# Optimization experiments

Hardware: AMD Instinct MI355X
Metric: run time of the kernel (lower is better)

The kernel has to match this reference:

```python
import jax, jax.numpy as jnp
import numpy as np

N, K, P_DIM, HID, NCLS = 20000, 16, 63, 32 + 0, 32
HID = 128
IN_DIM = P_DIM + 1


def setup_inputs() -> dict:
    key = jax.random.key(0)
    ks = iter(jax.random.split(key, 64))

    def nrm(shape, s=0.1):
        return jax.random.normal(next(ks), shape, jnp.float32) * s

    inp = {
        "p": nrm((N, P_DIM), 1.0),
        "neigh_idx": jax.random.randint(next(ks), (N, K), 0, N, dtype=jnp.int32),
    }
    dims = [(IN_DIM, HID), (HID, HID), (HID, NCLS)]
    for l, (din, dout) in enumerate(dims):
        inp[f"l{l}_Wih"] = nrm((4 * din, din))
        inp[f"l{l}_Whh"] = nrm((4 * din, din))
        inp[f"l{l}_bih"] = jnp.zeros((4 * din,), jnp.float32)
        inp[f"l{l}_bhh"] = jnp.zeros((4 * din,), jnp.float32)
        inp[f"l{l}_Wself"] = nrm((dout, din))
        inp[f"l{l}_Wneigh"] = nrm((dout, din))
        inp[f"l{l}_b"] = jnp.zeros((dout,), jnp.float32)
    return inp


def _lstm_agg(feat, neigh_idx, Wih, Whh, bih, bhh):
    # Per-node LSTM over the K in-neighbor features (DGL _lstm_reducer).
    n, h_dim = feat.shape[0], Whh.shape[1]
    bias = bih + bhh

    def step(carry, idx_t):
        h, c = carry
        x = feat[idx_t]                                   # [N, Din] gather (step t message)
        g = x @ Wih.T + h @ Whh.T + bias                  # [N, 4H]
        i, f, gg, o = jnp.split(g, 4, axis=-1)            # torch LSTM gate order i,f,g,o
        c = jax.nn.sigmoid(f) * c + jax.nn.sigmoid(i) * jnp.tanh(gg)
        h = jax.nn.sigmoid(o) * jnp.tanh(c)
        return (h, c), None

    init = (jnp.zeros((n, h_dim), feat.dtype), jnp.zeros((n, h_dim), feat.dtype))
    (h, _), _ = jax.lax.scan(step, init, neigh_idx.T)     # scan over K neighbor slots
    return h                                              # final hidden state = neigh feat


def _forward(p, neigh_idx, *params):
    # features = cat(in_degree/N, p); fixed-degree graph -> in_degree == K
    deg = jnp.full((p.shape[0], 1), K / N, p.dtype)
    feat = jnp.concatenate([deg, p], axis=1)
    layers = [params[7 * l: 7 * (l + 1)] for l in range(3)]
    for l, (Wih, Whh, bih, bhh, Wself, Wneigh, b) in enumerate(layers):
        neigh = _lstm_agg(feat, neigh_idx, Wih, Whh, bih, bhh)
        feat = feat @ Wself.T + neigh @ Wneigh.T + b      # fc_self + fc_neigh + bias
        if l < 2:
            feat = jax.nn.relu(feat)
    return feat


def reference(p, neigh_idx,
              l0_Wih, l0_Whh, l0_bih, l0_bhh, l0_Wself, l0_Wneigh, l0_b,
              l1_Wih, l1_Whh, l1_bih, l1_bhh, l1_Wself, l1_Wneigh, l1_b,
              l2_Wih, l2_Whh, l2_bih, l2_bhh, l2_Wself, l2_Wneigh, l2_b):
    return _forward(p, neigh_idx,
                    l0_Wih, l0_Whh, l0_bih, l0_bhh, l0_Wself, l0_Wneigh, l0_b,
                    l1_Wih, l1_Whh, l1_bih, l1_bhh, l1_Wself, l1_Wneigh, l1_b,
                    l2_Wih, l2_Whh, l2_bih, l2_bhh, l2_Wself, l2_Wneigh, l2_b)
```

## Files before the change

### kernel.cpp

```cpp
#include <hip/hip_runtime.h>
#include <hip/hip_bf16.h>
#include <stdint.h>


#define N_NODES 20000
#define KNE 16
#define C1F 1.442695041f
#define C2F 2.885390082f

typedef __bf16 bf16x8 __attribute__((ext_vector_type(8)));
typedef float f32x4 __attribute__((ext_vector_type(4)));

__device__ __forceinline__ bf16x8 ldb8(const __hip_bfloat16* p) {
  uint4 u = *reinterpret_cast<const uint4*>(p);
  return __builtin_bit_cast(bf16x8, u);
}
__device__ __forceinline__ void pin(bf16x8& v) {
  uint4 u = __builtin_bit_cast(uint4, v);
  asm volatile("" : "+v"(u.x), "+v"(u.y), "+v"(u.z), "+v"(u.w));
  v = __builtin_bit_cast(bf16x8, u);
}
__device__ __forceinline__ float b2f_lo(uint32_t u) {
  return __builtin_bit_cast(float, u << 16);
}
__device__ __forceinline__ float b2f_hi(uint32_t u) {
  return __builtin_bit_cast(float, u & 0xffff0000u);
}
__device__ __forceinline__ uint32_t pk2(float a, float b) {
  uint32_t ua = (uint32_t)__builtin_bit_cast(unsigned short, __float2bfloat16(a));
  uint32_t ub = (uint32_t)__builtin_bit_cast(unsigned short, __float2bfloat16(b));
  return ua | (ub << 16);
}

struct CvtArgs {
  const float* s[12];
  __hip_bfloat16* d[12];
  int off[13];
  int gsz[12];
};
__global__ void cvt_all(CvtArgs a) {
  int i = blockIdx.x * 256 + threadIdx.x;
  if (i >= a.off[12]) return;
#pragma unroll
  for (int k = 0; k < 12; ++k)
    if (i >= a.off[k] && i < a.off[k + 1]) {
      int j = i - a.off[k];
      float v = a.s[k][j];
      if (a.gsz[k]) {
        int g = j / a.gsz[k];
        v *= (g == 2) ? C2F : -C1F;
      }
      a.d[k][j] = __float2bfloat16(v);
    }
}

template <int DIN, int DOUT, int NTR, int WW>
__device__ __forceinline__ void proj_phase(
    const __hip_bfloat16* sA,
    const __hip_bfloat16* __restrict__ Wih,
    const float* __restrict__ bih, const float* __restrict__ bhh,
    const __hip_bfloat16* __restrict__ Wself,
    const float* __restrict__ bvec,
    __hip_bfloat16* __restrict__ P, float* __restrict__ S,
    int n0, int wv, int quad, int c16) {
  constexpr int KB = DIN / 32;
  constexpr int CCT = DIN / 16;
  constexpr int CTS = DOUT / 16;
  constexpr int HS = DIN + 8;
  const f32x4 zz = {0.f, 0.f, 0.f, 0.f};
  bf16x8 afr[NTR][KB];
#pragma unroll
  for (int nt = 0; nt < NTR; ++nt)
#pragma unroll
    for (int kb = 0; kb < KB; ++kb)
      afr[nt][kb] = ldb8(&sA[(nt * 16 + c16) * HS + kb * 32 + quad * 8]);

  for (int ct = wv; ct < CCT + CTS; ct += WW) {
    if (ct < CCT) {
      const int cc = ct * 16 + c16;
      f32x4 ag[4][NTR];
#pragma unroll
      for (int g = 0; g < 4; ++g)
#pragma unroll
        for (int nt = 0; nt < NTR; ++nt) ag[g][nt] = zz;
#pragma unroll
      for (int kb = 0; kb < KB; ++kb)
#pragma unroll
        for (int g = 0; g < 4; ++g) {
          bf16x8 b =
              ldb8(Wih + (size_t)(g * DIN + cc) * DIN + kb * 32 + quad * 8);
#pragma unroll
          for (int nt = 0; nt < NTR; ++nt)
            ag[g][nt] = __builtin_amdgcn_mfma_f32_16x16x32_bf16(
                afr[nt][kb], b, ag[g][nt], 0, 0, 0);
        }
      float bi = -C1F * (bih[cc] + bhh[cc]);
      float bf_ = -C1F * (bih[DIN + cc] + bhh[DIN + cc]);
      float bg = C2F * (bih[2 * DIN + cc] + bhh[2 * DIN + cc]);
      float bo = -C1F * (bih[3 * DIN + cc] + bhh[3 * DIN + cc]);
      uint2* Pp = reinterpret_cast<uint2*>(P);
#pragma unroll
      for (int nt = 0; nt < NTR; ++nt)
#pragma unroll
        for (int r = 0; r < 4; ++r) {
          int n = n0 + nt * 16 + quad * 4 + r;
          uint2 u;
          u.x = pk2(ag[0][nt][r] + bi, ag[1][nt][r] + bf_);
          u.y = pk2(ag[2][nt][r] + bg, ag[3][nt][r] + bo);
          Pp[(size_t)n * DIN + cc] = u;
        }
    } else {
      const int c = (ct - CCT) * 16 + c16;
      f32x4 a[NTR];
#pragma unroll
      for (int nt = 0; nt < NTR; ++nt) a[nt] = zz;
#pragma unroll
      for (int kb = 0; kb < KB; ++kb) {
        bf16x8 b = ldb8(Wself + (size_t)c * DIN + kb * 32 + quad * 8);
#pragma unroll
        for (int nt = 0; nt < NTR; ++nt)
          a[nt] = __builtin_amdgcn_mfma_f32_16x16x32_bf16(afr[nt][kb], b,
                                                          a[nt], 0, 0, 0);
      }
      float bias = bvec[c];
#pragma unroll
      for (int nt = 0; nt < NTR; ++nt)
#pragma unroll
        for (int r = 0; r < 4; ++r)
          S[(size_t)(n0 + nt * 16 + quad * 4 + r) * DOUT + c] =
              a[nt][r] + bias;
    }
  }
}

__global__ __launch_bounds__(256, 2) void feat_proj0(
    const float* __restrict__ p,
    const __hip_bfloat16* __restrict__ Wih,
    const float* __restrict__ bih, const float* __restrict__ bhh,
    const __hip_bfloat16* __restrict__ Wself,
    const float* __restrict__ bvec,
    __hip_bfloat16* __restrict__ P, float* __restrict__ S) {
  __shared__ __align__(16) __hip_bfloat16 sFeat[32 * 72];
  const int n0 = blockIdx.x * 32;
  const int tid = threadIdx.x;
  const int wv = tid >> 6;
  const int lane = tid & 63;
  const int quad = lane >> 4;
  const int c16 = lane & 15;

  for (int i = tid; i < 32 * 64; i += 256) {
    int n = i >> 6, c = i & 63;
    float v = (c == 0) ? ((float)KNE / (float)N_NODES)
                       : p[(size_t)(n0 + n) * 63 + c - 1];
    sFeat[n * 72 + c] = __float2bfloat16(v);
  }
  __syncthreads();
  proj_phase<64, 128, 2, 4>(sFeat, Wih, bih, bhh, Wself, bvec, P, S, n0, wv,
                            quad, c16);
}

template <int DIN, int DOUT, int DOUTN, int NT, bool RELU>
__global__ __launch_bounds__((DIN / 16) * 64)
__attribute__((amdgpu_waves_per_eu(4))) void lstm_proj_kern(
    const __hip_bfloat16* __restrict__ P,
    const float* __restrict__ S,
    const __hip_bfloat16* __restrict__ Whh,
    const __hip_bfloat16* __restrict__ Wng,
    const int* __restrict__ nidx,
    const __hip_bfloat16* __restrict__ Wih2,
    const float* __restrict__ bih2, const float* __restrict__ bhh2,
    const __hip_bfloat16* __restrict__ Wself2,
    const float* __restrict__ bvec2,
    __hip_bfloat16* __restrict__ P2, float* __restrict__ S2) {
  constexpr int W = DIN / 16;
  constexpr int KB = DIN / 32;
  constexpr int HS = DIN + 8;
  constexpr int NN = 16 * NT;
  constexpr int HS2 = DOUT + 8;

  __shared__ __align__(16) __hip_bfloat16 hl[2][NN * HS];
  __shared__ __align__(16) __hip_bfloat16 sOut[NN * HS2];
  __shared__ int idxl[NN * KNE];

  const int n0 = blockIdx.x * NN;
  const int tid = threadIdx.x;
  const int wv = tid >> 6;
  const int lane = tid & 63;
  const int quad = lane >> 4;
  const int c16 = lane & 15;
  const int col = wv * 16 + c16;

  for (int i = tid; i < NN * KNE; i += W * 64) idxl[i] = nidx[n0 * KNE + i];
  __syncthreads();

  uint2 pf[2][NT][4];
  auto loadpf = [&](int t, int b) {
#pragma unroll
    for (int nt = 0; nt < NT; ++nt)
#pragma unroll
      for (int r = 0; r < 4; ++r) {
        int src = idxl[(nt * 16 + quad * 4 + r) * KNE + t];
        pf[b][nt][r] =
            reinterpret_cast<const uint2*>(P + (size_t)src * (4 * DIN))[col];
      }
  };

  loadpf(0, 0);

  bf16x8 Bp[4][KB];
#pragma unroll
  for (int g = 0; g < 4; ++g)
#pragma unroll
    for (int kb = 0; kb < KB; ++kb) {
      Bp[g][kb] =
          ldb8(Whh + (size_t)(g * DIN + col) * DIN + kb * 32 + quad * 8);
      pin(Bp[g][kb]);
    }

  loadpf(1, 1);

  float cst[NT][4];
#pragma unroll
  for (int nt = 0; nt < NT; ++nt)
#pragma unroll
    for (int r = 0; r < 4; ++r) cst[nt][r] = 0.f;

  auto initag = [&](int b, int nt, f32x4 (&ag)[4]) {
#pragma unroll
    for (int r = 0; r < 4; ++r) {
      ag[0][r] = b2f_lo(pf[b][nt][r].x);
      ag[1][r] = b2f_hi(pf[b][nt][r].x);
      ag[2][r] = b2f_lo(pf[b][nt][r].y);
      ag[3][r] = b2f_hi(pf[b][nt][r].y);
    }
  };

  auto gates = [&](int hb, int nt, const f32x4 (&ag)[4]) {
#pragma unroll
    for (int r = 0; r < 4; ++r) {
      float wi = __builtin_amdgcn_rcpf(1.f + __builtin_amdgcn_exp2f(ag[0][r]));
      float wf = __builtin_amdgcn_rcpf(1.f + __builtin_amdgcn_exp2f(ag[1][r]));
      float wg = __builtin_amdgcn_rcpf(1.f + __builtin_amdgcn_exp2f(ag[2][r]));
      float wo = __builtin_amdgcn_rcpf(1.f + __builtin_amdgcn_exp2f(ag[3][r]));
      float tg = fmaf(-2.f, wg, 1.f);
      float cc = wf * cst[nt][r] + wi * tg;
      cst[nt][r] = cc;
      float tc = fmaf(
          -2.f,
          __builtin_amdgcn_rcpf(1.f + __builtin_amdgcn_exp2f(C2F * cc)), 1.f);
      hl[hb][(nt * 16 + quad * 4 + r) * HS + col] =
          __float2bfloat16(wo * tc);
    }
  };

#pragma unroll
  for (int nt = 0; nt < NT; ++nt) {
    f32x4 ag[4];
    initag(0, nt, ag);
    gates(0, nt, ag);
  }

#pragma unroll
  for (int t = 1; t < KNE; ++t) {
    __syncthreads();
    if (t + 1 < KNE) loadpf(t + 1, (t + 1) & 1);
    const int pb = (t - 1) & 1;
#pragma unroll
    for (int nt = 0; nt < NT; ++nt) {
      bf16x8 Af[KB];
#pragma unroll
      for (int kb = 0; kb < KB; ++kb)
        Af[kb] = ldb8(&hl[pb][(nt * 16 + c16) * HS + kb * 32 + quad * 8]);
      f32x4 ag[4];
      initag(t & 1, nt, ag);
#pragma unroll
      for (int kb = 0; kb < KB; ++kb)
#pragma unroll
        for (int g = 0; g < 4; ++g)
          ag[g] = __builtin_amdgcn_mfma_f32_16x16x32_bf16(Af[kb], Bp[g][kb],
                                                          ag[g], 0, 0, 0);
      gates(t & 1, nt, ag);
    }
  }

  const f32x4 zz = {0.f, 0.f, 0.f, 0.f};
  __syncthreads();
  bf16x8 Hf[NT][KB];
#pragma unroll
  for (int nt = 0; nt < NT; ++nt)
#pragma unroll
    for (int kb = 0; kb < KB; ++kb)
      Hf[nt][kb] = ldb8(&hl[1][(nt * 16 + c16) * HS + kb * 32 + quad * 8]);
  for (int ct = wv; ct < DOUT / 16; ct += W) {
    f32x4 a[NT];
#pragma unroll
    for (int nt = 0; nt < NT; ++nt) a[nt] = zz;
#pragma unroll
    for (int kb = 0; kb < KB; ++kb) {
      bf16x8 b = ldb8(Wng + (size_t)(ct * 16 + c16) * DIN + kb * 32 + quad * 8);
#pragma unroll
      for (int nt = 0; nt < NT; ++nt)
        a[nt] = __builtin_amdgcn_mfma_f32_16x16x32_bf16(Hf[nt][kb], b, a[nt],
                                                        0, 0, 0);
    }
#pragma unroll
    for (int nt = 0; nt < NT; ++nt)
#pragma unroll
      for (int r = 0; r < 4; ++r) {
        int n = n0 + nt * 16 + quad * 4 + r;
        int c = ct * 16 + c16;
        float v = a[nt][r] + S[(size_t)n * DOUT + c];
        if (RELU) v = fmaxf(v, 0.f);
        sOut[(nt * 16 + quad * 4 + r) * HS2 + c] = __float2bfloat16(v);
      }
  }
  __syncthreads();
  proj_phase<DOUT, DOUTN, NT, W>(sOut, Wih2, bih2, bhh2, Wself2, bvec2, P2,
                                 S2, n0, wv, quad, c16);
}

template <int DIN, int DOUT>
__global__ __launch_bounds__((DIN / 16) * 64)
__attribute__((amdgpu_waves_per_eu(4))) void lstm_out_kern(
    const __hip_bfloat16* __restrict__ P, const float* __restrict__ S,
    const __hip_bfloat16* __restrict__ Whh,
    const __hip_bfloat16* __restrict__ Wng, const int* __restrict__ nidx,
    float* __restrict__ outp) {
  constexpr int W = DIN / 16;
  constexpr int KB = DIN / 32;
  constexpr int HS = DIN + 8;

  __shared__ __align__(16) __hip_bfloat16 hl[2][16 * HS];
  __shared__ int idxl[16 * KNE];

  const int n0 = blockIdx.x * 16;
  const int tid = threadIdx.x;
  const int wv = tid >> 6;
  const int lane = tid & 63;
  const int quad = lane >> 4;
  const int c16 = lane & 15;
  const int col = wv * 16 + c16;

  for (int i = tid; i < 16 * KNE; i += W * 64) idxl[i] = nidx[n0 * KNE + i];
  __syncthreads();

  uint2 pf[2][4];
  auto loadpf = [&](int t, int b) {
#pragma unroll
    for (int r = 0; r < 4; ++r) {
      int src = idxl[(quad * 4 + r) * KNE + t];
      pf[b][r] =
          reinterpret_cast<const uint2*>(P + (size_t)src * (4 * DIN))[col];
    }
  };

  loadpf(0, 0);
  bf16x8 Bp[4][KB];
#pragma unroll
  for (int g = 0; g < 4; ++g)
#pragma unroll
    for (int kb = 0; kb < KB; ++kb) {
      Bp[g][kb] =
          ldb8(Whh + (size_t)(g * DIN + col) * DIN + kb * 32 + quad * 8);
      pin(Bp[g][kb]);
    }
  loadpf(1, 1);

  float cst[4];
#pragma unroll
  for (int r = 0; r < 4; ++r) cst[r] = 0.f;

  auto initag = [&](int b, f32x4 (&ag)[4]) {
#pragma unroll
    for (int r = 0; r < 4; ++r) {
      ag[0][r] = b2f_lo(pf[b][r].x);
      ag[1][r] = b2f_hi(pf[b][r].x);
      ag[2][r] = b2f_lo(pf[b][r].y);
      ag[3][r] = b2f_hi(pf[b][r].y);
    }
  };
  auto gates = [&](int hb, const f32x4 (&ag)[4]) {
#pragma unroll
    for (int r = 0; r < 4; ++r) {
      float wi = __builtin_amdgcn_rcpf(1.f + __builtin_amdgcn_exp2f(ag[0][r]));
      float wf = __builtin_amdgcn_rcpf(1.f + __builtin_amdgcn_exp2f(ag[1][r]));
      float wg = __builtin_amdgcn_rcpf(1.f + __builtin_amdgcn_exp2f(ag[2][r]));
      float wo = __builtin_amdgcn_rcpf(1.f + __builtin_amdgcn_exp2f(ag[3][r]));
      float tg = fmaf(-2.f, wg, 1.f);
      float cc = wf * cst[r] + wi * tg;
      cst[r] = cc;
      float tc = fmaf(
          -2.f,
          __builtin_amdgcn_rcpf(1.f + __builtin_amdgcn_exp2f(C2F * cc)), 1.f);
      hl[hb][(quad * 4 + r) * HS + col] = __float2bfloat16(wo * tc);
    }
  };

  {
    f32x4 ag[4];
    initag(0, ag);
    gates(0, ag);
  }
#pragma unroll
  for (int t = 1; t < KNE; ++t) {
    __syncthreads();
    if (t + 1 < KNE) loadpf(t + 1, (t + 1) & 1);
    const int pb = (t - 1) & 1;
    bf16x8 Af[KB];
#pragma unroll
    for (int kb = 0; kb < KB; ++kb)
      Af[kb] = ldb8(&hl[pb][c16 * HS + kb * 32 + quad * 8]);
    f32x4 ag[4];
    initag(t & 1, ag);
#pragma unroll
    for (int kb = 0; kb < KB; ++kb)
#pragma unroll
      for (int g = 0; g < 4; ++g)
        ag[g] = __builtin_amdgcn_mfma_f32_16x16x32_bf16(Af[kb], Bp[g][kb],
                                                        ag[g], 0, 0, 0);
    gates(t & 1, ag);
  }

  const f32x4 zz = {0.f, 0.f, 0.f, 0.f};
  __syncthreads();
  bf16x8 Hf[KB];
#pragma unroll
  for (int kb = 0; kb < KB; ++kb)
    Hf[kb] = ldb8(&hl[1][c16 * HS + kb * 32 + quad * 8]);
  for (int ct = wv; ct < DOUT / 16; ct += W) {
    f32x4 a = zz;
#pragma unroll
    for (int kb = 0; kb < KB; ++kb) {
      bf16x8 b = ldb8(Wng + (size_t)(ct * 16 + c16) * DIN + kb * 32 + quad * 8);
      a = __builtin_amdgcn_mfma_f32_16x16x32_bf16(Hf[kb], b, a, 0, 0, 0);
    }
#pragma unroll
    for (int r = 0; r < 4; ++r) {
      int n = n0 + quad * 4 + r;
      int c = ct * 16 + c16;
      outp[(size_t)n * DOUT + c] = a[r] + S[(size_t)n * DOUT + c];
    }
  }
}

extern "C" void kernel_launch(void* const* d_in, const int* in_sizes, int n_in,
                              void* d_out, int out_size, void* d_ws,
                              size_t ws_size, hipStream_t stream) {
  (void)in_sizes; (void)n_in; (void)out_size; (void)ws_size;
  const float* p = (const float*)d_in[0];
  const int* nidx = (const int*)d_in[1];
  const float* L[3][7];
  for (int l = 0; l < 3; ++l)
    for (int j = 0; j < 7; ++j)
      L[l][j] = (const float*)d_in[2 + 7 * l + j];

  char* w = (char*)d_ws;
  __hip_bfloat16* P0 = (__hip_bfloat16*)(w);
  float*          S0 = (float*)(w + 10240000);
  __hip_bfloat16* P1 = (__hip_bfloat16*)(w + 20480000);
  float*          S1 = (float*)(w + 40960000);
  float*          S2 = (float*)(w + 51200000);
  __hip_bfloat16* P2 = (__hip_bfloat16*)(w);
  __hip_bfloat16* wb = (__hip_bfloat16*)(w + 53760000);

  const int din_[3] = {64, 128, 128}, dout_[3] = {128, 128, 32};
  __hip_bfloat16 *Wih_b[3], *Whh_b[3], *Wself_b[3], *Wng_b[3];
  CvtArgs ca;
  size_t off = 0;
  int k = 0, pre = 0;
  for (int l = 0; l < 3; ++l) {
    int din = din_[l], dout = dout_[l];
    int n0 = 4 * din * din, n2 = dout * din;
    Wih_b[l] = wb + off;   off += (size_t)n0;
    Whh_b[l] = wb + off;   off += (size_t)n0;
    Wself_b[l] = wb + off; off += (size_t)n2;
    Wng_b[l] = wb + off;   off += (size_t)n2;
    const float* srcs[4] = {L[l][0], L[l][1], L[l][4], L[l][5]};
    __hip_bfloat16* dsts[4] = {Wih_b[l], Whh_b[l], Wself_b[l], Wng_b[l]};
    int ns[4] = {n0, n0, n2, n2};
    int gs[4] = {din * din, din * din, 0, 0};
    for (int j = 0; j < 4; ++j) {
      ca.s[k] = srcs[j];
      ca.d[k] = dsts[j];
      ca.off[k] = pre;
      ca.gsz[k] = gs[j];
      pre += ns[j];
      ++k;
    }
  }
  ca.off[12] = pre;

  cvt_all<<<(pre + 255) / 256, 256, 0, stream>>>(ca);

  feat_proj0<<<N_NODES / 32, 256, 0, stream>>>(
      p, Wih_b[0], L[0][2], L[0][3], Wself_b[0], L[0][6], P0, S0);

  lstm_proj_kern<64, 128, 128, 2, true><<<N_NODES / 32, 256, 0, stream>>>(
      P0, S0, Whh_b[0], Wng_b[0], nidx, Wih_b[1], L[1][2], L[1][3],
      Wself_b[1], L[1][6], P1, S1);

  lstm_proj_kern<128, 128, 32, 1, true><<<N_NODES / 16, 512, 0, stream>>>(
      P1, S1, Whh_b[1], Wng_b[1], nidx, Wih_b[2], L[2][2], L[2][3],
      Wself_b[2], L[2][6], P2, S2);

  lstm_out_kern<128, 32><<<N_NODES / 16, 512, 0, stream>>>(
      P2, S2, Whh_b[2], Wng_b[2], nidx, (float*)d_out);
}
```

Before: 327.3 us.

## Widen per-wave column tiles and stream Whh from cache in 128-dim LSTM kernels

```diff
diff --git a/kernel.cpp b/kernel.cpp
--- a/kernel.cpp
+++ b/kernel.cpp
@@ -159,8 +159,9 @@
                             quad, c16);
 }
 
-template <int DIN, int DOUT, int DOUTN, int NT, bool RELU>
-__global__ __launch_bounds__((DIN / 16) * 64)
+template <int DIN, int DOUT, int DOUTN, int NT, int CW, bool STREAMB,
+          bool RELU>
+__global__ __launch_bounds__((DIN / CW) * 64)
 __attribute__((amdgpu_waves_per_eu(4))) void lstm_proj_kern(
     const __hip_bfloat16* __restrict__ P,
     const float* __restrict__ S,
@@ -172,7 +173,8 @@
     const __hip_bfloat16* __restrict__ Wself2,
     const float* __restrict__ bvec2,
     __hip_bfloat16* __restrict__ P2, float* __restrict__ S2) {
-  constexpr int W = DIN / 16;
+  constexpr int W = DIN / CW;
+  constexpr int JJ = CW / 16;
   constexpr int KB = DIN / 32;
   constexpr int HS = DIN + 8;
   constexpr int NN = 16 * NT;
@@ -188,54 +190,63 @@
   const int lane = tid & 63;
   const int quad = lane >> 4;
   const int c16 = lane & 15;
-  const int col = wv * 16 + c16;
 
   for (int i = tid; i < NN * KNE; i += W * 64) idxl[i] = nidx[n0 * KNE + i];
   __syncthreads();
 
-  uint2 pf[2][NT][4];
+  uint2 pf[2][NT][JJ][4];
   auto loadpf = [&](int t, int b) {
 #pragma unroll
     for (int nt = 0; nt < NT; ++nt)
 #pragma unroll
       for (int r = 0; r < 4; ++r) {
         int src = idxl[(nt * 16 + quad * 4 + r) * KNE + t];
-        pf[b][nt][r] =
-            reinterpret_cast<const uint2*>(P + (size_t)src * (4 * DIN))[col];
+        const uint2* bp =
+            reinterpret_cast<const uint2*>(P + (size_t)src * (4 * DIN));
+#pragma unroll
+        for (int jj = 0; jj < JJ; ++jj)
+          pf[b][nt][jj][r] = bp[wv * CW + jj * 16 + c16];
       }
   };
 
   loadpf(0, 0);
 
-  bf16x8 Bp[4][KB];
-#pragma unroll
-  for (int g = 0; g < 4; ++g)
-#pragma unroll
-    for (int kb = 0; kb < KB; ++kb) {
-      Bp[g][kb] =
-          ldb8(Whh + (size_t)(g * DIN + col) * DIN + kb * 32 + quad * 8);
-      pin(Bp[g][kb]);
-    }
+  bf16x8 Bp[STREAMB ? 1 : 4][STREAMB ? 1 : JJ][STREAMB ? 1 : KB];
+  if constexpr (!STREAMB) {
+#pragma unroll
+    for (int g = 0; g < 4; ++g)
+#pragma unroll
+      for (int jj = 0; jj < JJ; ++jj)
+#pragma unroll
+        for (int kb = 0; kb < KB; ++kb) {
+          Bp[g][jj][kb] =
+              ldb8(Whh + (size_t)(g * DIN + wv * CW + jj * 16 + c16) * DIN +
+                   kb * 32 + quad * 8);
+          pin(Bp[g][jj][kb]);
+        }
+  }
 
   loadpf(1, 1);
 
-  float cst[NT][4];
+  float cst[NT][JJ][4];
 #pragma unroll
   for (int nt = 0; nt < NT; ++nt)
 #pragma unroll
-    for (int r = 0; r < 4; ++r) cst[nt][r] = 0.f;
-
-  auto initag = [&](int b, int nt, f32x4 (&ag)[4]) {
+    for (int jj = 0; jj < JJ; ++jj)
+#pragma unroll
+      for (int r = 0; r < 4; ++r) cst[nt][jj][r] = 0.f;
+
+  auto initag = [&](int b, int nt, int jj, f32x4 (&ag)[4]) {
 #pragma unroll
     for (int r = 0; r < 4; ++r) {
-      ag[0][r] = b2f_lo(pf[b][nt][r].x);
-      ag[1][r] = b2f_hi(pf[b][nt][r].x);
-      ag[2][r] = b2f_lo(pf[b][nt][r].y);
-      ag[3][r] = b2f_hi(pf[b][nt][r].y);
+      ag[0][r] = b2f_lo(pf[b][nt][jj][r].x);
+      ag[1][r] = b2f_hi(pf[b][nt][jj][r].x);
+      ag[2][r] = b2f_lo(pf[b][nt][jj][r].y);
+      ag[3][r] = b2f_hi(pf[b][nt][jj][r].y);
     }
   };
 
-  auto gates = [&](int hb, int nt, const f32x4 (&ag)[4]) {
+  auto gates = [&](int hb, int nt, int jj, const f32x4 (&ag)[4]) {
 #pragma unroll
     for (int r = 0; r < 4; ++r) {
       float wi = __builtin_amdgcn_rcpf(1.f + __builtin_amdgcn_exp2f(ag[0][r]));
@@ -243,43 +254,62 @@
       float wg = __builtin_amdgcn_rcpf(1.f + __builtin_amdgcn_exp2f(ag[2][r]));
       float wo = __builtin_amdgcn_rcpf(1.f + __builtin_amdgcn_exp2f(ag[3][r]));
       float tg = fmaf(-2.f, wg, 1.f);
-      float cc = wf * cst[nt][r] + wi * tg;
-      cst[nt][r] = cc;
+      float cc = wf * cst[nt][jj][r] + wi * tg;
+      cst[nt][jj][r] = cc;
       float tc = fmaf(
           -2.f,
           __builtin_amdgcn_rcpf(1.f + __builtin_amdgcn_exp2f(C2F * cc)), 1.f);
-      hl[hb][(nt * 16 + quad * 4 + r) * HS + col] =
+      hl[hb][(nt * 16 + quad * 4 + r) * HS + wv * CW + jj * 16 + c16] =
           __float2bfloat16(wo * tc);
     }
   };
 
 #pragma unroll
-  for (int nt = 0; nt < NT; ++nt) {
-    f32x4 ag[4];
-    initag(0, nt, ag);
-    gates(0, nt, ag);
-  }
+  for (int nt = 0; nt < NT; ++nt)
+#pragma unroll
+    for (int jj = 0; jj < JJ; ++jj) {
+      f32x4 ag[4];
+      initag(0, nt, jj, ag);
+      gates(0, nt, jj, ag);
+    }
 
 #pragma unroll
   for (int t = 1; t < KNE; ++t) {
     __syncthreads();
     if (t + 1 < KNE) loadpf(t + 1, (t + 1) & 1);
     const int pb = (t - 1) & 1;
+    const __hip_bfloat16* Wt = Whh;
+    if constexpr (STREAMB) {
+      int toff = 0;
+      asm volatile("" : "+s"(toff));
+      Wt = Whh + toff;
+    }
 #pragma unroll
     for (int nt = 0; nt < NT; ++nt) {
       bf16x8 Af[KB];
 #pragma unroll
       for (int kb = 0; kb < KB; ++kb)
         Af[kb] = ldb8(&hl[pb][(nt * 16 + c16) * HS + kb * 32 + quad * 8]);
-      f32x4 ag[4];
-      initag(t & 1, nt, ag);
-#pragma unroll
-      for (int kb = 0; kb < KB; ++kb)
-#pragma unroll
-        for (int g = 0; g < 4; ++g)
-          ag[g] = __builtin_amdgcn_mfma_f32_16x16x32_bf16(Af[kb], Bp[g][kb],
-                                                          ag[g], 0, 0, 0);
-      gates(t & 1, nt, ag);
+#pragma unroll
+      for (int jj = 0; jj < JJ; ++jj) {
+        f32x4 ag[4];
+        initag(t & 1, nt, jj, ag);
+#pragma unroll
+        for (int kb = 0; kb < KB; ++kb)
+#pragma unroll
+          for (int g = 0; g < 4; ++g) {
+            bf16x8 b;
+            if constexpr (STREAMB)
+              b = ldb8(Wt +
+                       (size_t)(g * DIN + wv * CW + jj * 16 + c16) * DIN +
+                       kb * 32 + quad * 8);
+            else
+              b = Bp[g][jj][kb];
+            ag[g] = __builtin_amdgcn_mfma_f32_16x16x32_bf16(Af[kb], b, ag[g],
+                                                            0, 0, 0);
+          }
+        gates(t & 1, nt, jj, ag);
+      }
     }
   }
 
@@ -319,14 +349,15 @@
                                  S2, n0, wv, quad, c16);
 }
 
-template <int DIN, int DOUT>
-__global__ __launch_bounds__((DIN / 16) * 64)
+template <int DIN, int DOUT, int CW, bool STREAMB>
+__global__ __launch_bounds__((DIN / CW) * 64)
 __attribute__((amdgpu_waves_per_eu(4))) void lstm_out_kern(
     const __hip_bfloat16* __restrict__ P, const float* __restrict__ S,
     const __hip_bfloat16* __restrict__ Whh,
     const __hip_bfloat16* __restrict__ Wng, const int* __restrict__ nidx,
     float* __restrict__ outp) {
-  constexpr int W = DIN / 16;
+  constexpr int W = DIN / CW;
+  constexpr int JJ = CW / 16;
   constexpr int KB = DIN / 32;
   constexpr int HS = DIN + 8;
 
@@ -339,47 +370,58 @@
   const int lane = tid & 63;
   const int quad = lane >> 4;
   const int c16 = lane & 15;
-  const int col = wv * 16 + c16;
 
   for (int i = tid; i < 16 * KNE; i += W * 64) idxl[i] = nidx[n0 * KNE + i];
   __syncthreads();
 
-  uint2 pf[2][4];
+  uint2 pf[2][JJ][4];
   auto loadpf = [&](int t, int b) {
 #pragma unroll
     for (int r = 0; r < 4; ++r) {
       int src = idxl[(quad * 4 + r) * KNE + t];
-      pf[b][r] =
-          reinterpret_cast<const uint2*>(P + (size_t)src * (4 * DIN))[col];
+      const uint2* bp =
+          reinterpret_cast<const uint2*>(P + (size_t)src * (4 * DIN));
+#pragma unroll
+      for (int jj = 0; jj < JJ; ++jj)
+        pf[b][jj][r] = bp[wv * CW + jj * 16 + c16];
     }
   };
 
   loadpf(0, 0);
-  bf16x8 Bp[4][KB];
-#pragma unroll
-  for (int g = 0; g < 4; ++g)
-#pragma unroll
-    for (int kb = 0; kb < KB; ++kb) {
-      Bp[g][kb] =
-          ldb8(Whh + (size_t)(g * DIN + col) * DIN + kb * 32 + quad * 8);
-      pin(Bp[g][kb]);
-    }
+
+  bf16x8 Bp[STREAMB ? 1 : 4][STREAMB ? 1 : JJ][STREAMB ? 1 : KB];
+  if constexpr (!STREAMB) {
+#pragma unroll
+    for (int g = 0; g < 4; ++g)
+#pragma unroll
+      for (int jj = 0; jj < JJ; ++jj)
+#pragma unroll
+        for (int kb = 0; kb < KB; ++kb) {
+          Bp[g][jj][kb] =
+              ldb8(Whh + (size_t)(g * DIN + wv * CW + jj * 16 + c16) * DIN +
+                   kb * 32 + quad * 8);
+          pin(Bp[g][jj][kb]);
+        }
+  }
+
   loadpf(1, 1);
 
-  float cst[4];
-#pragma unroll
-  for (int r = 0; r < 4; ++r) cst[r] = 0.f;
-
-  auto initag = [&](int b, f32x4 (&ag)[4]) {
+  float cst[JJ][4];
+#pragma unroll
+  for (int jj = 0; jj < JJ; ++jj)
+#pragma unroll
+    for (int r = 0; r < 4; ++r) cst[jj][r] = 0.f;
+
+  auto initag = [&](int b, int jj, f32x4 (&ag)[4]) {
 #pragma unroll
     for (int r = 0; r < 4; ++r) {
-      ag[0][r] = b2f_lo(pf[b][r].x);
-      ag[1][r] = b2f_hi(pf[b][r].x);
-      ag[2][r] = b2f_lo(pf[b][r].y);
-      ag[3][r] = b2f_hi(pf[b][r].y);
+      ag[0][r] = b2f_lo(pf[b][jj][r].x);
+      ag[1][r] = b2f_hi(pf[b][jj][r].x);
+      ag[2][r] = b2f_lo(pf[b][jj][r].y);
+      ag[3][r] = b2f_hi(pf[b][jj][r].y);
     }
   };
-  auto gates = [&](int hb, const f32x4 (&ag)[4]) {
+  auto gates = [&](int hb, int jj, const f32x4 (&ag)[4]) {
 #pragma unroll
     for (int r = 0; r < 4; ++r) {
       float wi = __builtin_amdgcn_rcpf(1.f + __builtin_amdgcn_exp2f(ag[0][r]));
@@ -387,38 +429,57 @@
       float wg = __builtin_amdgcn_rcpf(1.f + __builtin_amdgcn_exp2f(ag[2][r]));
       float wo = __builtin_amdgcn_rcpf(1.f + __builtin_amdgcn_exp2f(ag[3][r]));
       float tg = fmaf(-2.f, wg, 1.f);
-      float cc = wf * cst[r] + wi * tg;
-      cst[r] = cc;
+      float cc = wf * cst[jj][r] + wi * tg;
+      cst[jj][r] = cc;
       float tc = fmaf(
           -2.f,
           __builtin_amdgcn_rcpf(1.f + __builtin_amdgcn_exp2f(C2F * cc)), 1.f);
-      hl[hb][(quad * 4 + r) * HS + col] = __float2bfloat16(wo * tc);
+      hl[hb][(quad * 4 + r) * HS + wv * CW + jj * 16 + c16] =
+          __float2bfloat16(wo * tc);
     }
   };
 
-  {
+#pragma unroll
+  for (int jj = 0; jj < JJ; ++jj) {
     f32x4 ag[4];
-    initag(0, ag);
-    gates(0, ag);
-  }
+    initag(0, jj, ag);
+    gates(0, jj, ag);
+  }
+
 #pragma unroll
   for (int t = 1; t < KNE; ++t) {
     __syncthreads();
     if (t + 1 < KNE) loadpf(t + 1, (t + 1) & 1);
     const int pb = (t - 1) & 1;
+    const __hip_bfloat16* Wt = Whh;
+    if constexpr (STREAMB) {
+      int toff = 0;
+      asm volatile("" : "+s"(toff));
+      Wt = Whh + toff;
+    }
     bf16x8 Af[KB];
 #pragma unroll
     for (int kb = 0; kb < KB; ++kb)
       Af[kb] = ldb8(&hl[pb][c16 * HS + kb * 32 + quad * 8]);
-    f32x4 ag[4];
-    initag(t & 1, ag);
-#pragma unroll
-    for (int kb = 0; kb < KB; ++kb)
-#pragma unroll
-      for (int g = 0; g < 4; ++g)
-        ag[g] = __builtin_amdgcn_mfma_f32_16x16x32_bf16(Af[kb], Bp[g][kb],
-                                                        ag[g], 0, 0, 0);
-    gates(t & 1, ag);
+#pragma unroll
+    for (int jj = 0; jj < JJ; ++jj) {
+      f32x4 ag[4];
+      initag(t & 1, jj, ag);
+#pragma unroll
+      for (int kb = 0; kb < KB; ++kb)
+#pragma unroll
+        for (int g = 0; g < 4; ++g) {
+          bf16x8 b;
+          if constexpr (STREAMB)
+            b = ldb8(Wt + (size_t)(g * DIN + wv * CW + jj * 16 + c16) * DIN +
+                     kb * 32 + quad * 8);
+          else
+            b = Bp[g][jj][kb];
+          ag[g] = __builtin_amdgcn_mfma_f32_16x16x32_bf16(Af[kb], b, ag[g],
+                                                          0, 0, 0);
+        }
+      gates(t & 1, jj, ag);
+    }
   }
 
   const f32x4 zz = {0.f, 0.f, 0.f, 0.f};
@@ -495,14 +556,16 @@
   feat_proj0<<<N_NODES / 32, 256, 0, stream>>>(
       p, Wih_b[0], L[0][2], L[0][3], Wself_b[0], L[0][6], P0, S0);
 
-  lstm_proj_kern<64, 128, 128, 2, true><<<N_NODES / 32, 256, 0, stream>>>(
-      P0, S0, Whh_b[0], Wng_b[0], nidx, Wih_b[1], L[1][2], L[1][3],
-      Wself_b[1], L[1][6], P1, S1);
-
-  lstm_proj_kern<128, 128, 32, 1, true><<<N_NODES / 16, 512, 0, stream>>>(
-      P1, S1, Whh_b[1], Wng_b[1], nidx, Wih_b[2], L[2][2], L[2][3],
-      Wself_b[2], L[2][6], P2, S2);
-
-  lstm_out_kern<128, 32><<<N_NODES / 16, 512, 0, stream>>>(
+  lstm_proj_kern<64, 128, 128, 2, 16, false, true>
+      <<<N_NODES / 32, 256, 0, stream>>>(P0, S0, Whh_b[0], Wng_b[0], nidx,
+                                         Wih_b[1], L[1][2], L[1][3],
+                                         Wself_b[1], L[1][6], P1, S1);
+
+  lstm_proj_kern<128, 128, 32, 1, 32, true, true>
+      <<<N_NODES / 16, 256, 0, stream>>>(P1, S1, Whh_b[1], Wng_b[1], nidx,
+                                         Wih_b[2], L[2][2], L[2][3],
+                                         Wself_b[2], L[2][6], P2, S2);
+
+  lstm_out_kern<128, 32, 32, true><<<N_NODES / 16, 256, 0, stream>>>(
       P2, S2, Whh_b[2], Wng_b[2], nidx, (float*)d_out);
 }
```

After: 879.9 us. 2.69x slower.
